# Optimization experiments

Hardware: AMD Instinct MI355X
Metric: run time of the kernel (lower is better)

The kernel has to match this reference:

```python
import jax, jax.numpy as jnp
import numpy as np

B, C, H, W = 8, 6, 512, 512
N_SIGMA = 1
NUM_CLASS = 3
RES = 256
FG_W = 1.0
MAX_ID = 16  # instance ids in [0, 16); 0 is background
W_INST, W_VAR, W_SEED = 1.0, 10.0, 1.0
GAMMA = 2.0


def make_xym():
    ym = jnp.broadcast_to(jnp.linspace(0.0, H // RES, H)[None, :, None], (1, H, W))
    xm = jnp.broadcast_to(jnp.linspace(0.0, W // RES, W)[None, None, :], (1, H, W))
    return jnp.concatenate([xm, ym], 0)  # (2, H, W), channel 0 = x, 1 = y


def lovasz_hinge_flat(logits, labels_f):
    # logits, labels_f: (P,) ; labels in {0,1}
    signs = 2.0 * labels_f - 1.0
    errors = 1.0 - logits * signs
    order = jnp.argsort(-errors)  # descending
    errors_sorted = errors[order]
    gt_sorted = labels_f[order]
    gts = gt_sorted.sum()
    intersection = gts - jnp.cumsum(gt_sorted)
    union = gts + jnp.cumsum(1.0 - gt_sorted)
    jaccard = 1.0 - intersection / union
    grad = jaccard.at[1:].set(jaccard[1:] - jaccard[:-1])
    grad = jax.lax.stop_gradient(grad)
    return jnp.sum(jax.nn.relu(errors_sorted) * grad)


def focal_loss_multiclass(logits, target):
    # logits: (B, NUM_CLASS, H, W), target: (B, H, W) int class ids
    logpt = jax.nn.log_softmax(logits, axis=1)
    lp = jnp.take_along_axis(logpt, target[:, None], axis=1)[:, 0]  # (B,H,W)
    pt = jnp.exp(lp)
    return jnp.mean(-((1.0 - pt) ** GAMMA) * lp)


def setup_inputs() -> dict:
    key = jax.random.key(0)
    k1, k2, k3 = jax.random.split(key, 3)
    prediction = jax.random.normal(k1, (B, C, H, W), dtype=jnp.float32)
    labels = jax.random.randint(k2, (B, NUM_CLASS, H, W), 0, 2, dtype=jnp.int32)
    instances = jax.random.randint(k3, (B, 1, H, W), 0, MAX_ID, dtype=jnp.int32)
    return {"prediction": prediction, "labels": labels, "instances": instances}


def _loss(prediction, labels, instances):
    xym = make_xym()
    ids = jnp.arange(1, MAX_ID)

    def per_image(pred_b, inst_b, lab_b):
        spatial_emb = jnp.tanh(pred_b[0:2]) + xym           # (2,H,W)
        sigma = pred_b[2]                                    # (H,W), n_sigma=1
        seed = jax.nn.sigmoid(pred_b[2 + N_SIGMA + NUM_CLASS - 1])  # (H,W)
        label_fg = lab_b[-1]                                 # (H,W)
        bg_seed = jnp.sum(jnp.where(label_fg == 0, seed ** 2, 0.0))

        def per_id(k):
            mask = (inst_b[0] == k).astype(pred_b.dtype)     # (H,W)
            cnt = mask.sum()
            safe = jnp.maximum(cnt, 1.0)
            center = (xym * mask).sum((1, 2)) / safe         # (2,) to_center=True
            s_mean = (sigma * mask).sum() / safe
            var = (mask * (sigma - jax.lax.stop_gradient(s_mean)) ** 2).sum() / safe
            s = jnp.exp(s_mean * 10.0)
            dist = jnp.exp(-s * ((spatial_emb - center[:, None, None]) ** 2).sum(0))
            lov = lovasz_hinge_flat((dist * 2.0 - 1.0).ravel(), mask.ravel())
            seed_fg = FG_W * (mask * (seed - jax.lax.stop_gradient(dist)) ** 2).sum()
            return cnt > 0, lov, var, seed_fg

        valid, lov, var, sfg = jax.vmap(per_id)(ids)
        nobj = jnp.maximum(valid.sum().astype(pred_b.dtype), 1.0)
        inst_loss = jnp.where(valid, lov, 0.0).sum() / nobj
        var_loss = jnp.where(valid, var, 0.0).sum() / nobj
        seed_loss = (bg_seed + jnp.where(valid, sfg, 0.0).sum()) / (H * W)
        return W_INST * inst_loss + W_VAR * var_loss + W_SEED * seed_loss

    per_b = jax.vmap(per_image)(prediction, instances, labels)
    binary_closs = focal_loss_multiclass(
        prediction[:, 2 + N_SIGMA:2 + N_SIGMA + NUM_CLASS],
        jnp.argmax(labels, axis=1))
    return jnp.mean(per_b) + binary_closs


def reference(prediction, labels, instances):
    return _loss(prediction, labels, instances)
```

## Files before the change

### kernel.cpp

```cpp
#include <hip/hip_runtime.h>
#include <math.h>

#define BB 8
#define HWH (512*512)
#define NID 15
#define NSEG (BB*NID)
#define NBINS 256
#define AAF ((float)NBINS/13.0f)
#define LOG2E 1.442695041f
#define LN2 0.6931471806f

typedef unsigned int uint32;
typedef unsigned long long uint64;

__device__ __forceinline__ float ftanh(float x){
    float t = __expf(2.0f*x);
    return 1.0f - 2.0f*__builtin_amdgcn_rcpf(t + 1.0f);
}
__device__ __forceinline__ float fsigmoid(float x){
    return __builtin_amdgcn_rcpf(1.0f + __expf(-x));
}
__device__ __forceinline__ float sconst(float x){
    return __uint_as_float(__builtin_amdgcn_readfirstlane(__float_as_uint(x)));
}

__global__ __launch_bounds__(256, 8) void phase1f(const float* __restrict__ pred,
        const int* __restrict__ labels, const int* __restrict__ inst,
        uint64* __restrict__ pstat64, float* __restrict__ pstatf,
        float* __restrict__ pstatf2,
        float* __restrict__ bgseed_p, float* __restrict__ focal_p){
    int blk = blockIdx.x;
    int b = blk >> 8;
    int t = threadIdx.x;
    int q = (blk & 255)*256 + t;

    __shared__ uint64 s64[NID];
    __shared__ float ssig[NID], ssig2[NID];
    __shared__ float wfb[4][2];
    if (t < NID){ s64[t] = 0ull; ssig[t] = 0.0f; ssig2[t] = 0.0f; }
    __syncthreads();

    const int Q = HWH/4;
    const float4* P = (const float4*)(pred + (size_t)b*6*HWH);
    const int4* L = (const int4*)(labels + (size_t)b*3*HWH);
    const int4* I = (const int4*)(inst + (size_t)b*HWH);
    float4 sg4 = P[2*Q+q], z3 = P[3*Q+q], z4 = P[4*Q+q], z5 = P[5*Q+q];
    int4 id4 = I[q];
    int4 l0 = L[q], l1 = L[Q+q], l2 = L[2*Q+q];
    int p = q*4;
    int w0 = p & 511, h0 = p >> 9;

    float facc = 0.0f, bacc = 0.0f;
    auto px = [&](float sgv, float z3v, float z4v, float z5v, int id,
                  int L0, int L1, int L2, int wv){
        float seed = fsigmoid(z5v);
        if (L2 == 0) bacc += seed*seed;
        int tc = 0, best = L0;
        if (L1 > best){ tc = 1; best = L1; }
        if (L2 > best){ tc = 2; }
        float m = fmaxf(z3v, fmaxf(z4v, z5v));
        float e3 = __expf(z3v-m), e4 = __expf(z4v-m), e5 = __expf(z5v-m);
        float sum = e3+e4+e5;
        float lse = m + __logf(sum);
        float zt = (tc==0) ? z3v : ((tc==1) ? z4v : z5v);
        float et = (tc==0) ? e3  : ((tc==1) ? e4  : e5);
        float lp = zt - lse;
        float pt = et*__builtin_amdgcn_rcpf(sum);
        float om = 1.0f - pt;
        facc -= om*om*lp;
        if (id > 0){
            atomicAdd(&s64[id-1],
                      (1ull<<42) | ((uint64)(uint32)wv<<21) | (uint64)(uint32)h0);
            atomicAdd(&ssig[id-1], sgv);
            atomicAdd(&ssig2[id-1], sgv*sgv);
        }
    };
    px(sg4.x, z3.x, z4.x, z5.x, id4.x, l0.x, l1.x, l2.x, w0);
    px(sg4.y, z3.y, z4.y, z5.y, id4.y, l0.y, l1.y, l2.y, w0+1);
    px(sg4.z, z3.z, z4.z, z5.z, id4.z, l0.z, l1.z, l2.z, w0+2);
    px(sg4.w, z3.w, z4.w, z5.w, id4.w, l0.w, l1.w, l2.w, w0+3);

    for (int o = 32; o; o >>= 1){
        facc += __shfl_xor(facc, o);
        bacc += __shfl_xor(bacc, o);
    }
    if ((t & 63) == 0){ wfb[t>>6][0] = facc; wfb[t>>6][1] = bacc; }
    __syncthreads();
    if (t < NID){
        pstat64[blk*16 + t] = s64[t];
        pstatf [blk*16 + t] = ssig[t];
        pstatf2[blk*16 + t] = ssig2[t];
    }
    if (t == 0){
        focal_p[blk]  = wfb[0][0]+wfb[1][0]+wfb[2][0]+wfb[3][0];
        bgseed_p[blk] = wfb[0][1]+wfb[1][1]+wfb[2][1]+wfb[3][1];
    }
}

__global__ __launch_bounds__(512) void phaseR(const uint64* __restrict__ pstat64,
        const float* __restrict__ pstatf, const float* __restrict__ pstatf2,
        const float* __restrict__ focal_p, const float* __restrict__ bgseed_p,
        float* __restrict__ stats, float* __restrict__ derived,
        float* __restrict__ results,
        float* __restrict__ focalR, float* __restrict__ bgseedR){
    int b = blockIdx.x;
    int t = threadIdx.x;
    int k = t & 15, chunk = t >> 4;
    float acnt = 0, asw = 0, ash = 0, af = 0, af2 = 0;
    for (int i = 0; i < 8; i++){
        int blk = b*256 + chunk*8 + i;
        uint64 v = pstat64[blk*16 + k];
        acnt += (float)(uint32)(v >> 42);
        asw  += (float)(uint32)((v >> 21) & 0x1FFFFF);
        ash  += (float)(uint32)(v & 0x1FFFFF);
        af   += pstatf[blk*16 + k];
        af2  += pstatf2[blk*16 + k];
    }
    __shared__ float tc[16], tw[16], th[16], ts[16], ts2[16];
    if (t < 16){ tc[t]=0; tw[t]=0; th[t]=0; ts[t]=0; ts2[t]=0; }
    __syncthreads();
    atomicAdd(&tc[k], acnt);
    atomicAdd(&tw[k], asw);
    atomicAdd(&th[k], ash);
    atomicAdd(&ts[k], af);
    atomicAdd(&ts2[k], af2);
    __syncthreads();
    if (t < NID){
        float cnt = tc[t];
        float safe = fmaxf(cnt, 1.0f);
        float inv = 1.0f/safe;
        const float SC = 2.0f/511.0f;
        derived[(b*NID+t)*4+0] = tw[t]*SC*inv;
        derived[(b*NID+t)*4+1] = th[t]*SC*inv;
        float sm = ts[t]*inv;
        derived[(b*NID+t)*4+2] = __expf(10.0f*sm);
        derived[(b*NID+t)*4+3] = sm;
        stats[b*60 + t*4] = cnt;
        results[(size_t)(b*NID+t)*3 + 1] = ts2[t] - cnt*sm*sm;
    }
    int w = t >> 6, lane = t & 63;
    if (w == 0){
        float f = 0;
        for (int j = 0; j < 4; j++) f += focal_p[b*256 + j*64 + lane];
        for (int o = 32; o; o >>= 1) f += __shfl_xor(f, o);
        if (lane == 0) focalR[b] = f;
    } else if (w == 1){
        float g = 0;
        for (int j = 0; j < 4; j++) g += bgseed_p[b*256 + j*64 + lane];
        for (int o = 32; o; o >>= 1) g += __shfl_xor(g, o);
        if (lane == 0) bgseedR[b] = g;
    }
}

__global__ __launch_bounds__(512, 8) void phaseLH(const float* __restrict__ pred,
        const int* __restrict__ inst, const float* __restrict__ derived,
        uint32* __restrict__ part, float* __restrict__ part2, int S){
    int idx = blockIdx.x;
    int b = idx & 7;
    int sp = idx >> 3;
    int t = threadIdx.x;
    int lane = t & 63;

    __shared__ __align__(16) uint32 hist[NID*NBINS];
    __shared__ float ssl[NID];
    __shared__ float vsB[NID];
    {
        uint4* hz = (uint4*)hist;
        for (int i = t; i < NID*NBINS/4; i += 512) hz[i] = make_uint4(0,0,0,0);
    }
    if (t < NID){
        ssl[t] = derived[(size_t)(b*NID + t)*4 + 2];
        vsB[t] = 0.0f;
    }
    float kcx[NID], kcy[NID], kcs[NID];
    #pragma unroll
    for (int j = 0; j < NID; j++){
        const float* d0 = derived + (size_t)(b*NID + j)*4;
        kcx[j] = sconst(d0[0]);
        kcy[j] = sconst(d0[1]);
        kcs[j] = sconst(LOG2E*AAF*d0[2]);
    }
    __syncthreads();

    const int Q = HWH/4;
    int qps = Q / S;
    int q0 = sp * qps;
    const float* pb = pred + (size_t)b*6*HWH;
    const float4* P0 = (const float4*)pb;
    const float4* P1 = P0 + Q;
    const float* z5p = pb + 5*HWH;
    const int4* I = (const int4*)(inst + (size_t)b*HWH);
    const float SC = 2.0f/511.0f;

    for (int q = q0 + t; q < q0 + qps; q += 512){
        int4 id4 = I[q];
        float4 a = P0[q], c = P1[q];
        int p = q*4;
        float gx = (float)(p & 511)*SC;
        float gy = (float)(p >> 9)*SC;
        auto px = [&](float av, float cv, int id, float gxv, int pi){
            float ex = ftanh(av) + gxv;
            float ey = ftanh(cv) + gy;
            int own = id - 1;
            float r2own = 0.0f;
            #pragma unroll
            for (int j = 0; j < NID; j++){
                float dx = ex - kcx[j], dy = ey - kcy[j];
                float r2 = fmaf(dx, dx, dy*dy);
                if (j == own) r2own = r2;
                float binf = fmaf(-kcs[j], r2, (float)NBINS);
                binf = fminf(fmaxf(binf, 0.0f), (float)(NBINS-1));
                int bin = (int)binf;
                bool isown = (j == own);
                bool hot = (bin == 0) && !isown;
                uint64 bal = __ballot(hot);
                if (hot){
                    if ((bal & ((1ull << lane) - 1ull)) == 0ull)
                        atomicAdd(&hist[j*NBINS],
                                  ((uint32)__popcll(bal)) << 16);
                } else if (!isown){
                    atomicAdd(&hist[j*NBINS + bin], 65536u);
                }
            }
            if (own >= 0){
                float d = __expf(-ssl[own]*r2own);
                float e = fmaf(-2.0f, d, 2.0f);
                float bf = fmaf(__log2f(e), AAF, (float)NBINS - AAF);
                bf = fminf(fmaxf(bf, 0.0f), (float)(NBINS-1));
                atomicAdd(&hist[own*NBINS + (int)bf], 65537u);
                float seed = fsigmoid(z5p[pi]);
                float sd = seed - d;
                atomicAdd(&vsB[own], sd*sd);
            }
        };
        px(a.x, c.x, id4.x, gx,      p);
        px(a.y, c.y, id4.y, gx+SC,   p+1);
        px(a.z, c.z, id4.z, gx+2*SC, p+2);
        px(a.w, c.w, id4.w, gx+3*SC, p+3);
    }
    __syncthreads();
    uint4* dst = (uint4*)(part + (size_t)(b*S + sp)*NID*NBINS);
    const uint4* hs = (const uint4*)hist;
    for (int i = t; i < NID*NBINS/4; i += 512) dst[i] = hs[i];
    if (t < NID) part2[(size_t)(b*S + sp)*NID + t] = vsB[t];
}

__global__ __launch_bounds__(256) void phaseM(const uint32* __restrict__ part,
        uint32* __restrict__ part_m, int S){
    int idx = blockIdx.x;
    int b = idx & 7;
    int r = idx >> 3;
    int k = r % NID;
    int g = r / NID;
    int t = threadIdx.x;
    int spn = S >> 3;
    uint32 acc = 0;
    for (int i = 0; i < spn; i++){
        const uint32* src = part + ((size_t)(b*S + g*spn + i)*NID + k)*NBINS;
        acc += src[t];
    }
    part_m[((size_t)(b*8 + g)*NID + k)*NBINS + t] = acc;
}

__global__ __launch_bounds__(256) void phaseLS(const uint32* __restrict__ part_m,
        const float* __restrict__ part2, const float* __restrict__ stats,
        float* __restrict__ results, int S){
    int idx = blockIdx.x;
    int b = idx & 7, k = idx >> 3;
    int seg = b*NID + k;
    int t = threadIdx.x;

    __shared__ uint32 hc[NBINS], hg[NBINS];
    __shared__ uint32 wbc[4], wbg[4], wexc[4], wexg[4];
    __shared__ float wsum[4];

    uint32 c = 0, g = 0;
    for (int gi = 0; gi < 8; gi++){
        uint32 v = part_m[((size_t)(b*8 + gi)*NID + k)*NBINS + t];
        c += v >> 16; g += v & 0xFFFFu;
    }
    hc[t] = c; hg[t] = g;
    __syncthreads();

    uint32 cd = hc[NBINS-1-t], gd = hg[NBINS-1-t];
    uint32 ci = cd, gi2 = gd;
    int lane = t & 63, w = t >> 6;
    for (int o = 1; o < 64; o <<= 1){
        uint32 cu = __shfl_up(ci, o);
        uint32 gu = __shfl_up(gi2, o);
        if (lane >= o){ ci += cu; gi2 += gu; }
    }
    if (lane == 63){ wbc[w] = ci; wbg[w] = gi2; }
    __syncthreads();
    if (t == 0){
        uint32 rc = 0, rg = 0;
        for (int i = 0; i < 4; i++){
            uint32 a = wbc[i], bq = wbg[i];
            wexc[i] = rc; wexg[i] = rg;
            rc += a; rg += bq;
        }
    }
    __syncthreads();

    float G = stats[b*60 + k*4];
    float contrib = 0.0f;
    if (G > 0.0f && (cd | gd)){
        uint32 nb = wexc[w] + (ci - cd);
        uint32 gb = wexg[w] + (gi2 - gd);
        float jp = 0.0f;
        if (nb > 0) jp = 1.0f - (G - (float)gb)/(G + (float)(nb - gb));
        uint32 n = nb + cd, gg = gb + gd;
        float j2 = 1.0f - (G - (float)gg)/(G + (float)(n - gg));
        int bin = NBINS-1-t;
        float ev = __expf(LN2*(((float)bin + 0.5f)*(13.0f/(float)NBINS) - 12.0f));
        contrib = ev*(j2 - jp);
    }
    for (int o = 32; o; o >>= 1) contrib += __shfl_xor(contrib, o);
    if ((t & 63) == 0) wsum[w] = contrib;
    __syncthreads();
    if (t == 0)
        results[(size_t)seg*3 + 0] = wsum[0]+wsum[1]+wsum[2]+wsum[3];
    if (w == 1){
        float ss = 0.0f;
        for (int sp = lane; sp < S; sp += 64)
            ss += part2[(size_t)(b*S + sp)*NID + k];
        for (int o = 32; o; o >>= 1) ss += __shfl_xor(ss, o);
        if (lane == 0) results[(size_t)seg*3 + 2] = ss;
    }
}

__global__ void phase5(const float* __restrict__ stats, const float* __restrict__ results,
                       const float* __restrict__ bgseedR, const float* __restrict__ focalR,
                       float* __restrict__ out){
    int t = threadIdx.x;
    __shared__ float per_b[BB];
    if (t < BB){
        float nvalid = 0.0f, lsum = 0.0f, vsum = 0.0f, ssum = 0.0f;
        for (int k = 0; k < NID; k++){
            int seg = t*NID + k;
            float cnt = stats[t*60 + k*4];
            if (cnt > 0.0f){
                nvalid += 1.0f;
                lsum += results[seg*3+0];
                vsum += results[seg*3+1]/cnt;
                ssum += results[seg*3+2];
            }
        }
        float nobj = fmaxf(nvalid, 1.0f);
        per_b[t] = lsum/nobj + 10.0f*(vsum/nobj) + (bgseedR[t] + ssum)/(float)HWH;
    }
    __syncthreads();
    if (t == 0){
        float s = 0.0f, fs = 0.0f;
        for (int b = 0; b < BB; b++){ s += per_b[b]; fs += focalR[b]; }
        out[0] = s/(float)BB + fs/(float)(BB*HWH);
    }
}

extern "C" void kernel_launch(void* const* d_in, const int* in_sizes, int n_in,
                              void* d_out, int out_size, void* d_ws, size_t ws_size,
                              hipStream_t stream){
    const float* pred  = (const float*)d_in[0];
    const int*   labels= (const int*)d_in[1];
    const int*   inst  = (const int*)d_in[2];
    float* out = (float*)d_out;

    auto need = [](int S){
        return (size_t)BB*S*NID*NBINS*4ull
             + (size_t)120*8*NBINS*4ull
             + (size_t)BB*S*NID*4ull
             + 2048ull*16*8 + 2048ull*16*4*2
             + 2048ull*4*2
             + (480+480+360+16)*4ull;
    };
    int S = 16;
    if      (ws_size >= need(128)) S = 128;
    else if (ws_size >= need(64))  S = 64;
    else if (ws_size >= need(32))  S = 32;

    uint32* part   = (uint32*)d_ws;
    uint32* part_m = part + (size_t)BB*S*NID*NBINS;
    float* part2   = (float*)(part_m + (size_t)120*8*NBINS);
    uint64* pstat64= (uint64*)(part2 + (size_t)BB*S*NID);
    float* pstatf  = (float*)(pstat64 + 2048*16);
    float* pstatf2 = pstatf + 2048*16;
    float* focal_p = pstatf2 + 2048*16;
    float* bgseed_p= focal_p + 2048;
    float* stats   = bgseed_p + 2048;
    float* derived = stats + 480;
    float* results = derived + 480;
    float* focalR  = results + 360;
    float* bgseedR = focalR + 8;

    hipLaunchKernelGGL(phase1f, dim3(2048), dim3(256), 0, stream,
                       pred, labels, inst, pstat64, pstatf, pstatf2, bgseed_p, focal_p);
    hipLaunchKernelGGL(phaseR, dim3(8), dim3(512), 0, stream,
                       pstat64, pstatf, pstatf2, focal_p, bgseed_p,
                       stats, derived, results, focalR, bgseedR);
    hipLaunchKernelGGL(phaseLH, dim3(BB*S), dim3(512), 0, stream,
                       pred, inst, derived, part, part2, S);
    hipLaunchKernelGGL(phaseM, dim3(960), dim3(256), 0, stream, part, part_m, S);
    hipLaunchKernelGGL(phaseLS, dim3(NSEG), dim3(256), 0, stream,
                       part_m, part2, stats, results, S);
    hipLaunchKernelGGL(phase5, dim3(1), dim3(64), 0, stream,
                       stats, results, bgseedR, focalR, out);
}
```

Before: 80.64 us.

## Merge per-slice histograms with global atomics and drop the merge kernel

```diff
diff --git a/kernel.cpp b/kernel.cpp
--- a/kernel.cpp
+++ b/kernel.cpp
@@ -9,6 +9,7 @@
 #define AAF ((float)NBINS/13.0f)
 #define LOG2E 1.442695041f
 #define LN2 0.6931471806f
+#define SLICES 128
 
 typedef unsigned int uint32;
 typedef unsigned long long uint64;
@@ -102,9 +103,17 @@
         const float* __restrict__ focal_p, const float* __restrict__ bgseed_p,
         float* __restrict__ stats, float* __restrict__ derived,
         float* __restrict__ results,
-        float* __restrict__ focalR, float* __restrict__ bgseedR){
+        float* __restrict__ focalR, float* __restrict__ bgseedR,
+        uint32* __restrict__ Hzero, float* __restrict__ part2f){
     int b = blockIdx.x;
     int t = threadIdx.x;
+
+    {
+        const int stripe = 2*NSEG*NBINS/8;
+        for (int i = b*stripe + t; i < (b+1)*stripe; i += 512) Hzero[i] = 0u;
+        if (b == 0 && t < NSEG) part2f[t] = 0.0f;
+    }
+
     int k = t & 15, chunk = t >> 4;
     float acnt = 0, asw = 0, ash = 0, af = 0, af2 = 0;
     for (int i = 0; i < 8; i++){
@@ -154,7 +163,8 @@
 
 __global__ __launch_bounds__(512, 8) void phaseLH(const float* __restrict__ pred,
         const int* __restrict__ inst, const float* __restrict__ derived,
-        uint32* __restrict__ part, float* __restrict__ part2, int S){
+        uint32* __restrict__ Hc, uint32* __restrict__ Hg,
+        float* __restrict__ part2f){
     int idx = blockIdx.x;
     int b = idx & 7;
     int sp = idx >> 3;
@@ -183,7 +193,7 @@
     __syncthreads();
 
     const int Q = HWH/4;
-    int qps = Q / S;
+    const int qps = Q / SLICES;
     int q0 = sp * qps;
     const float* pb = pred + (size_t)b*6*HWH;
     const float4* P0 = (const float4*)pb;
@@ -239,50 +249,33 @@
         px(a.w, c.w, id4.w, gx+3*SC, p+3);
     }
     __syncthreads();
-    uint4* dst = (uint4*)(part + (size_t)(b*S + sp)*NID*NBINS);
-    const uint4* hs = (const uint4*)hist;
-    for (int i = t; i < NID*NBINS/4; i += 512) dst[i] = hs[i];
-    if (t < NID) part2[(size_t)(b*S + sp)*NID + t] = vsB[t];
-}
-
-__global__ __launch_bounds__(256) void phaseM(const uint32* __restrict__ part,
-        uint32* __restrict__ part_m, int S){
-    int idx = blockIdx.x;
-    int b = idx & 7;
-    int r = idx >> 3;
-    int k = r % NID;
-    int g = r / NID;
-    int t = threadIdx.x;
-    int spn = S >> 3;
-    uint32 acc = 0;
-    for (int i = 0; i < spn; i++){
-        const uint32* src = part + ((size_t)(b*S + g*spn + i)*NID + k)*NBINS;
-        acc += src[t];
-    }
-    part_m[((size_t)(b*8 + g)*NID + k)*NBINS + t] = acc;
-}
-
-__global__ __launch_bounds__(256) void phaseLS(const uint32* __restrict__ part_m,
-        const float* __restrict__ part2, const float* __restrict__ stats,
-        float* __restrict__ results, int S){
+    size_t base = (size_t)b*NID*NBINS;
+    for (int i = t; i < NID*NBINS; i += 512){
+        uint32 v = hist[i];
+        if (v){
+            uint32 cc = v >> 16, gg = v & 0xFFFFu;
+            if (cc) atomicAdd(&Hc[base + i], cc);
+            if (gg) atomicAdd(&Hg[base + i], gg);
+        }
+    }
+    if (t < NID && vsB[t] != 0.0f)
+        atomicAdd(&part2f[b*NID + t], vsB[t]);
+}
+
+__global__ __launch_bounds__(256) void phaseLS(const uint32* __restrict__ Hc,
+        const uint32* __restrict__ Hg, const float* __restrict__ part2f,
+        const float* __restrict__ stats, float* __restrict__ results){
     int idx = blockIdx.x;
     int b = idx & 7, k = idx >> 3;
     int seg = b*NID + k;
     int t = threadIdx.x;
 
-    __shared__ uint32 hc[NBINS], hg[NBINS];
     __shared__ uint32 wbc[4], wbg[4], wexc[4], wexg[4];
     __shared__ float wsum[4];
 
-    uint32 c = 0, g = 0;
-    for (int gi = 0; gi < 8; gi++){
-        uint32 v = part_m[((size_t)(b*8 + gi)*NID + k)*NBINS + t];
-        c += v >> 16; g += v & 0xFFFFu;
-    }
-    hc[t] = c; hg[t] = g;
-    __syncthreads();
-
-    uint32 cd = hc[NBINS-1-t], gd = hg[NBINS-1-t];
+    size_t base = (size_t)seg*NBINS;
+    uint32 cd = Hc[base + NBINS-1-t];
+    uint32 gd = Hg[base + NBINS-1-t];
     uint32 ci = cd, gi2 = gd;
     int lane = t & 63, w = t >> 6;
     for (int o = 1; o < 64; o <<= 1){
@@ -318,14 +311,9 @@
     for (int o = 32; o; o >>= 1) contrib += __shfl_xor(contrib, o);
     if ((t & 63) == 0) wsum[w] = contrib;
     __syncthreads();
-    if (t == 0)
+    if (t == 0){
         results[(size_t)seg*3 + 0] = wsum[0]+wsum[1]+wsum[2]+wsum[3];
-    if (w == 1){
-        float ss = 0.0f;
-        for (int sp = lane; sp < S; sp += 64)
-            ss += part2[(size_t)(b*S + sp)*NID + k];
-        for (int o = 32; o; o >>= 1) ss += __shfl_xor(ss, o);
-        if (lane == 0) results[(size_t)seg*3 + 2] = ss;
+        results[(size_t)seg*3 + 2] = part2f[seg];
     }
 }
 
@@ -365,23 +353,10 @@
     const int*   inst  = (const int*)d_in[2];
     float* out = (float*)d_out;
 
-    auto need = [](int S){
-        return (size_t)BB*S*NID*NBINS*4ull
-             + (size_t)120*8*NBINS*4ull
-             + (size_t)BB*S*NID*4ull
-             + 2048ull*16*8 + 2048ull*16*4*2
-             + 2048ull*4*2
-             + (480+480+360+16)*4ull;
-    };
-    int S = 16;
-    if      (ws_size >= need(128)) S = 128;
-    else if (ws_size >= need(64))  S = 64;
-    else if (ws_size >= need(32))  S = 32;
-
-    uint32* part   = (uint32*)d_ws;
-    uint32* part_m = part + (size_t)BB*S*NID*NBINS;
-    float* part2   = (float*)(part_m + (size_t)120*8*NBINS);
-    uint64* pstat64= (uint64*)(part2 + (size_t)BB*S*NID);
+    uint32* Hc     = (uint32*)d_ws;
+    uint32* Hg     = Hc + (size_t)NSEG*NBINS;
+    float* part2f  = (float*)(Hg + (size_t)NSEG*NBINS);
+    uint64* pstat64= (uint64*)(part2f + NSEG);
     float* pstatf  = (float*)(pstat64 + 2048*16);
     float* pstatf2 = pstatf + 2048*16;
     float* focal_p = pstatf2 + 2048*16;
@@ -396,12 +371,11 @@
                        pred, labels, inst, pstat64, pstatf, pstatf2, bgseed_p, focal_p);
     hipLaunchKernelGGL(phaseR, dim3(8), dim3(512), 0, stream,
                        pstat64, pstatf, pstatf2, focal_p, bgseed_p,
-                       stats, derived, results, focalR, bgseedR);
-    hipLaunchKernelGGL(phaseLH, dim3(BB*S), dim3(512), 0, stream,
-                       pred, inst, derived, part, part2, S);
-    hipLaunchKernelGGL(phaseM, dim3(960), dim3(256), 0, stream, part, part_m, S);
+                       stats, derived, results, focalR, bgseedR, Hc, part2f);
+    hipLaunchKernelGGL(phaseLH, dim3(BB*SLICES), dim3(512), 0, stream,
+                       pred, inst, derived, Hc, Hg, part2f);
     hipLaunchKernelGGL(phaseLS, dim3(NSEG), dim3(256), 0, stream,
-                       part_m, part2, stats, results, S);
+                       Hc, Hg, part2f, stats, results);
     hipLaunchKernelGGL(phase5, dim3(1), dim3(64), 0, stream,
                        stats, results, bgseedR, focalR, out);
 }
```

New measurement: 78.46 us. 2.7% less time.
